# Kernel optimization log

Hardware: AMD Instinct MI355X
Metric: run time of the kernel (lower is better)

Reference implementation:

```python
import jax, jax.numpy as jnp
import numpy as np

RES = 512
N_LAYERS = 3
BATCH = 128
NUM_CLASSES = 10
LAMBDA = 5.32e-07
K = 2.0 * np.pi / LAMBDA  # module-level constant k in the original code
Z = 0.035                 # propagation distance d
DX = 1e-06                # pixel pitch


def _transfer_function(res):
    # Angular-spectrum Fresnel transfer function H(fx, fy), static numpy precompute.
    fx = np.fft.fftfreq(res, DX)
    FX, FY = np.meshgrid(fx, fx)
    H = np.exp(1j * K * Z) * np.exp(-1j * np.pi * LAMBDA * Z * (FX ** 2 + FY ** 2))
    return jnp.asarray(H.astype(np.complex64))


def setup_inputs() -> dict:
    key = jax.random.key(0)
    k1, k2, k3, k4 = jax.random.split(key, 4)
    x = jax.random.normal(k1, (BATCH, 1, RES, RES), dtype=jnp.float32)
    phases = jax.random.normal(k2, (N_LAYERS, RES, RES), dtype=jnp.float32) * 0.1
    fc_w = jax.random.normal(k3, (NUM_CLASSES, RES * RES), dtype=jnp.float32) * 0.01
    fc_b = jax.random.normal(k4, (NUM_CLASSES,), dtype=jnp.float32) * 0.01
    return {"x": x, "phases": phases, "fc_w": fc_w, "fc_b": fc_b}


def reference(x, phases, fc_w, fc_b):
    res = x.shape[-1]
    H = _transfer_function(res)  # (res, res) complex64
    field = x[:, 0].astype(jnp.complex64)  # (B, res, res)
    for i in range(phases.shape[0]):
        # phase-mask multiply, then Fresnel propagation: ifft2(fft2(field) * H)
        field = field * jnp.exp(1j * phases[i])
        field = jnp.fft.ifft2(jnp.fft.fft2(field, axes=(-2, -1)) * H, axes=(-2, -1))
    intensity = field.real ** 2 + field.imag ** 2  # |field|^2
    feat = intensity.reshape(x.shape[0], -1)
    return feat @ fc_w.T + fc_b
```

## Files before the change

### kernel.cpp

```cpp
#include <hip/hip_runtime.h>
#include <math.h>


#define PAD(i) ((i) + ((i) >> 4))
#define LSTR 545
#define PSTR 545

typedef __attribute__((ext_vector_type(2))) _Float16 half2v;
typedef __attribute__((ext_vector_type(8))) _Float16 half8;

__device__ __forceinline__ void wave_lds_order() {
  asm volatile("" ::: "memory");
}

__device__ __forceinline__ float2 cadd(float2 a, float2 b){ return make_float2(a.x+b.x, a.y+b.y); }
__device__ __forceinline__ float2 csub(float2 a, float2 b){ return make_float2(a.x-b.x, a.y-b.y); }
__device__ __forceinline__ float2 cmul(float2 a, float2 b){ return make_float2(a.x*b.x - a.y*b.y, a.x*b.y + a.y*b.x); }

template<int S>
__device__ __forceinline__ float2 cmul_s(float2 a, float2 b) {
  return (S < 0) ? make_float2(a.x*b.x - a.y*b.y, a.x*b.y + a.y*b.x)
                 : make_float2(a.x*b.x + a.y*b.y, a.y*b.x - a.x*b.y);
}

template<int S>
__device__ __forceinline__ float2 crot(float2 z){
  return (S > 0) ? make_float2(-z.y, z.x) : make_float2(z.y, -z.x);
}

template<int S>
__device__ __forceinline__ void fft8(float2 v[8]) {
  const float sq = 0.70710678118654752440f;
  float2 t0 = cadd(v[0], v[4]), t1 = csub(v[0], v[4]);
  float2 t2 = cadd(v[2], v[6]), t3 = csub(v[2], v[6]);
  float2 E0 = cadd(t0, t2), E2 = csub(t0, t2);
  float2 rt3 = crot<S>(t3);
  float2 E1 = cadd(t1, rt3), E3 = csub(t1, rt3);
  float2 u0 = cadd(v[1], v[5]), u1 = csub(v[1], v[5]);
  float2 u2 = cadd(v[3], v[7]), u3 = csub(v[3], v[7]);
  float2 O0 = cadd(u0, u2), O2 = csub(u0, u2);
  float2 ru3 = crot<S>(u3);
  float2 O1 = cadd(u1, ru3), O3 = csub(u1, ru3);
  float2 O1w = make_float2(sq*(O1.x - (float)S*O1.y), sq*((float)S*O1.x + O1.y));
  float2 O2w = crot<S>(O2);
  float2 O3w = make_float2(-sq*(O3.x + (float)S*O3.y), sq*((float)S*O3.x - O3.y));
  v[0] = cadd(E0, O0);  v[4] = csub(E0, O0);
  v[1] = cadd(E1, O1w); v[5] = csub(E1, O1w);
  v[2] = cadd(E2, O2w); v[6] = csub(E2, O2w);
  v[3] = cadd(E3, O3w); v[7] = csub(E3, O3w);
}

__device__ __forceinline__ void mktw(float2 tw2[7], float2 tw3[7], int t) {
  float a2 = -6.28318530717958647692f * (float)(t & 7) / 64.0f;
  float a3 = -6.28318530717958647692f * (float)(t & 63) / 512.0f;
  float s2, c2; __sincosf(a2, &s2, &c2);
  float s3, c3; __sincosf(a3, &s3, &c3);
  float2 w2 = make_float2(c2, s2), w3 = make_float2(c3, s3);
  tw2[0] = w2; tw3[0] = w3;
  #pragma unroll
  for (int r = 1; r < 7; ++r) { tw2[r] = cmul(tw2[r-1], w2); tw3[r] = cmul(tw3[r-1], w3); }
}

template<int S>
__device__ __forceinline__ void fft512_w(float2 v[8], float2* __restrict__ B, int t,
                                         const float2 tw2[7], const float2 tw3[7]) {
  fft8<S>(v);
  #pragma unroll
  for (int r = 0; r < 8; ++r) B[PAD(8*t + r)] = v[r];
  wave_lds_order();
  #pragma unroll
  for (int r = 0; r < 8; ++r) v[r] = B[PAD(t + 64*r)];
  #pragma unroll
  for (int r = 1; r < 8; ++r) v[r] = cmul_s<S>(v[r], tw2[r-1]);
  fft8<S>(v);
  int d = ((t >> 3) << 6) | (t & 7);
  #pragma unroll
  for (int r = 0; r < 8; ++r) B[PAD(d + 8*r)] = v[r];
  wave_lds_order();
  #pragma unroll
  for (int r = 0; r < 8; ++r) v[r] = B[PAD(t + 64*r)];
  #pragma unroll
  for (int r = 1; r < 8; ++r) v[r] = cmul_s<S>(v[r], tw3[r-1]);
  fft8<S>(v);
}

template<int S>
__device__ __forceinline__ void fft512_pair(float2 vA[8], float2 vB[8],
                                            float4* __restrict__ B, int t,
                                            const float2 tw2[7], const float2 tw3[7]) {
  fft8<S>(vA); fft8<S>(vB);
  #pragma unroll
  for (int r = 0; r < 8; ++r)
    B[PAD(8*t + r)] = make_float4(vA[r].x, vA[r].y, vB[r].x, vB[r].y);
  wave_lds_order();
  #pragma unroll
  for (int r = 0; r < 8; ++r) {
    float4 w = B[PAD(t + 64*r)];
    vA[r] = make_float2(w.x, w.y); vB[r] = make_float2(w.z, w.w);
  }
  #pragma unroll
  for (int r = 1; r < 8; ++r) {
    vA[r] = cmul_s<S>(vA[r], tw2[r-1]); vB[r] = cmul_s<S>(vB[r], tw2[r-1]);
  }
  fft8<S>(vA); fft8<S>(vB);
  int d = ((t >> 3) << 6) | (t & 7);
  #pragma unroll
  for (int r = 0; r < 8; ++r)
    B[PAD(d + 8*r)] = make_float4(vA[r].x, vA[r].y, vB[r].x, vB[r].y);
  wave_lds_order();
  #pragma unroll
  for (int r = 0; r < 8; ++r) {
    float4 w = B[PAD(t + 64*r)];
    vA[r] = make_float2(w.x, w.y); vB[r] = make_float2(w.z, w.w);
  }
  #pragma unroll
  for (int r = 1; r < 8; ++r) {
    vA[r] = cmul_s<S>(vA[r], tw3[r-1]); vB[r] = cmul_s<S>(vB[r], tw3[r-1]);
  }
  fft8<S>(vA); fft8<S>(vB);
}

__device__ __forceinline__ float2 h2f(half2v h) { return make_float2((float)h[0], (float)h[1]); }
__device__ __forceinline__ half2v f2h(float2 v) { half2v h; h[0] = (_Float16)v.x; h[1] = (_Float16)v.y; return h; }


__global__ __launch_bounds__(256) void k_hinit(float2* __restrict__ hx,
                                               float2* __restrict__ hy) {
  int idx = blockIdx.x * 256 + threadIdx.x;
  int u = idx & 511;
  double f = (double)(u < 256 ? u : u - 512) * 1953.125;
  const double LAM = 5.32e-7, ZD = 0.035;
  const double PI = 3.14159265358979323846;
  double s, c;
  if (idx < 512) {
    double ang = -PI * LAM * ZD * f * f;
    sincos(ang, &s, &c);
    hx[u] = make_float2((float)c, (float)s);
  } else {
    double ang = (2.0 * PI / LAM) * ZD - PI * LAM * ZD * f * f;
    sincos(ang, &s, &c);
    const double sc = 1.0 / 262144.0;
    hy[u] = make_float2((float)(c * sc), (float)(s * sc));
  }
}

__global__ __launch_bounds__(256) void k_r1(const float* __restrict__ x,
                                            const float* __restrict__ ph,
                                            half2v* __restrict__ F) {
  __shared__ float2 lds[4 * LSTR];
  int tid = threadIdx.x;
  int t = tid & 63, rl = tid >> 6;
  size_t row = (size_t)blockIdx.x * 4 + rl;
  int y = (int)(row & 511);
  const float* xr = x + row * 512;
  const float* pr = ph + (size_t)y * 512;
  float2 tw2[7], tw3[7];
  mktw(tw2, tw3, t);
  float2 v[8];
  #pragma unroll
  for (int r = 0; r < 8; ++r) {
    int e = t + 64*r;
    float a = xr[e];
    float p = pr[e];
    float sn, cs; __sincosf(p, &sn, &cs);
    v[r] = make_float2(a * cs, a * sn);
  }
  fft512_w<-1>(v, lds + rl * LSTR, t, tw2, tw3);
  half2v* Fr = F + row * 512;
  #pragma unroll
  for (int r = 0; r < 8; ++r) Fr[t + 64*r] = f2h(v[r]);
}

__global__ __launch_bounds__(256) void k_rmid(half2v* __restrict__ F,
                                              const float* __restrict__ ph) {
  __shared__ float2 lds[4 * LSTR];
  int tid = threadIdx.x;
  int t = tid & 63, rl = tid >> 6;
  size_t row = (size_t)blockIdx.x * 4 + rl;
  int y = (int)(row & 511);
  half2v* Fr = F + row * 512;
  const float* pr = ph + (size_t)y * 512;
  float pv[8];
  #pragma unroll
  for (int r = 0; r < 8; ++r) pv[r] = pr[t + 64*r];
  float2 tw2[7], tw3[7];
  mktw(tw2, tw3, t);
  float2 v[8];
  #pragma unroll
  for (int r = 0; r < 8; ++r) v[r] = h2f(Fr[t + 64*r]);
  fft512_w<1>(v, lds + rl * LSTR, t, tw2, tw3);
  #pragma unroll
  for (int r = 0; r < 8; ++r) {
    float sn, cs; __sincosf(pv[r], &sn, &cs);
    v[r] = cmul(v[r], make_float2(cs, sn));
  }
  fft512_w<-1>(v, lds + rl * LSTR, t, tw2, tw3);
  #pragma unroll
  for (int r = 0; r < 8; ++r) Fr[t + 64*r] = f2h(v[r]);
}

__global__ __launch_bounds__(512) void k_col(half2v* __restrict__ F,
                                             const float2* __restrict__ hx,
                                             const float2* __restrict__ hy) {
  __shared__ float4 lds[8 * PSTR];
  int b = blockIdx.x >> 5;
  int x0 = (blockIdx.x & 31) << 4;
  half2v* Fb = F + (size_t)b * 262144;
  half8* Fb8 = (half8*)Fb;
  int tid = threadIdx.x;
  int t = tid & 63, cl = tid >> 6;
  float2 hyv[8];
  #pragma unroll
  for (int r = 0; r < 8; ++r) hyv[r] = hy[t + 64*r];
  float2 hxA = hx[x0 + 2*cl], hxB = hx[x0 + 2*cl + 1];
  float2 tw2[7], tw3[7];
  mktw(tw2, tw3, t);
  #pragma unroll
  for (int i = 0; i < 4; ++i) {
    int f = tid + 512 * i;
    int yy = f >> 2, c4 = f & 3;
    half8 d = Fb8[(size_t)yy * 128 + (x0 >> 2) + c4];
    int pb = PAD(yy);
    lds[(2*c4)     * PSTR + pb] = make_float4((float)d[0], (float)d[1],
                                              (float)d[2], (float)d[3]);
    lds[(2*c4 + 1) * PSTR + pb] = make_float4((float)d[4], (float)d[5],
                                              (float)d[6], (float)d[7]);
  }
  __syncthreads();
  float4* B = lds + cl * PSTR;
  float2 vA[8], vB[8];
  #pragma unroll
  for (int r = 0; r < 8; ++r) {
    float4 w = B[PAD(t + 64*r)];
    vA[r] = make_float2(w.x, w.y); vB[r] = make_float2(w.z, w.w);
  }
  fft512_pair<-1>(vA, vB, B, t, tw2, tw3);
  #pragma unroll
  for (int r = 0; r < 8; ++r) {
    vA[r] = cmul(cmul(vA[r], hyv[r]), hxA);
    vB[r] = cmul(cmul(vB[r], hyv[r]), hxB);
  }
  fft512_pair<1>(vA, vB, B, t, tw2, tw3);
  #pragma unroll
  for (int r = 0; r < 8; ++r)
    B[PAD(t + 64*r)] = make_float4(vA[r].x, vA[r].y, vB[r].x, vB[r].y);
  __syncthreads();
  #pragma unroll
  for (int i = 0; i < 4; ++i) {
    int f = tid + 512 * i;
    int yy = f >> 2, c4 = f & 3;
    int pb = PAD(yy);
    float4 a  = lds[(2*c4)     * PSTR + pb];
    float4 bb = lds[(2*c4 + 1) * PSTR + pb];
    half8 o;
    o[0] = (_Float16)a.x;  o[1] = (_Float16)a.y;
    o[2] = (_Float16)a.z;  o[3] = (_Float16)a.w;
    o[4] = (_Float16)bb.x; o[5] = (_Float16)bb.y;
    o[6] = (_Float16)bb.z; o[7] = (_Float16)bb.w;
    Fb8[(size_t)yy * 128 + (x0 >> 2) + c4] = o;
  }
}

__global__ __launch_bounds__(256) void k_rlast(const half2v* __restrict__ F,
                                               const float* __restrict__ W,
                                               float* __restrict__ partial, int m) {
  __shared__ float2 lds[4 * LSTR];
  int tid = threadIdx.x;
  int t = tid & 63, rl = tid >> 6;
  int nq = (m + 3) >> 2;
  int y = blockIdx.x / nq;
  int q = blockIdx.x - y * nq;
  int g = q * 4 + rl;
  bool act = (g < m);
  const half2v* Fr = F + ((size_t)g * 262144 + (size_t)y * 512);
  float2 tw2[7], tw3[7];
  mktw(tw2, tw3, t);
  float2 v[8];
  #pragma unroll
  for (int r = 0; r < 8; ++r) {
    half2v h = act ? Fr[t + 64*r] : (half2v)(_Float16)0.0f;
    v[r] = h2f(h);
  }
  fft512_w<1>(v, lds + rl * LSTR, t, tw2, tw3);
  float acc[10];
  #pragma unroll
  for (int c = 0; c < 10; ++c) acc[c] = 0.0f;
  const float* Wy = W + (size_t)y * 512;
  #pragma unroll
  for (int r = 0; r < 8; ++r) {
    int e = t + 64*r;
    float I = v[r].x * v[r].x + v[r].y * v[r].y;
    #pragma unroll
    for (int c = 0; c < 10; ++c) acc[c] += I * Wy[(size_t)c * 262144 + e];
  }
  float mine = 0.0f;
  #pragma unroll
  for (int c = 0; c < 10; ++c) {
    float s = acc[c];
    #pragma unroll
    for (int off = 32; off > 0; off >>= 1) s += __shfl_xor(s, off, 64);
    if (t == c) mine = s;
  }
  if (act && t < 10)
    partial[((size_t)g * 10 + t) * 512 + y] = mine;
}

__global__ __launch_bounds__(64) void k_fc(const float* __restrict__ partial,
                                           const float* __restrict__ fc_b,
                                           float* __restrict__ out, int b0, int m) {
  int bid = blockIdx.x;
  int g = bid / 10, c = bid - g * 10;
  int t = threadIdx.x;
  const float* p = partial + ((size_t)g * 10 + c) * 512;
  float s = 0.0f;
  #pragma unroll
  for (int r = 0; r < 8; ++r) s += p[t + 64*r];
  #pragma unroll
  for (int off = 32; off > 0; off >>= 1) s += __shfl_xor(s, off, 64);
  if (t == 0) out[(size_t)(b0 + g) * 10 + c] = s + fc_b[c];
}


extern "C" void kernel_launch(void* const* d_in, const int* in_sizes, int n_in,
                              void* d_out, int out_size, void* d_ws, size_t ws_size,
                              hipStream_t stream) {
  const float* x    = (const float*)d_in[0];
  const float* ph   = (const float*)d_in[1];
  const float* fc_w = (const float*)d_in[2];
  const float* fc_b = (const float*)d_in[3];
  float* out = (float*)d_out;

  const size_t IMG = 262144;
  const size_t PER_IMG = IMG * sizeof(half2v) + 512 * 10 * sizeof(float);
  float2* hx = (float2*)d_ws;
  float2* hy = hx + 512;
  size_t avail = (ws_size > IMG * sizeof(float2)) ? ws_size - IMG * sizeof(float2) : 0;
  int M = (int)(avail / PER_IMG);
  if (M < 1) M = 1;
  if (M > 128) M = 128;
  half2v* F  = (half2v*)((char*)d_ws + IMG * sizeof(float2));
  float* part = (float*)((char*)F + (size_t)M * IMG * sizeof(half2v));

  hipLaunchKernelGGL(k_hinit, dim3(4), dim3(256), 0, stream, hx, hy);

  for (int b0 = 0; b0 < 128; b0 += M) {
    int m = (128 - b0 < M) ? (128 - b0) : M;
    int rblocks = m * 128;
    int cblocks = m * 32;
    int nq = (m + 3) >> 2;
    hipLaunchKernelGGL(k_r1,    dim3(rblocks), dim3(256), 0, stream, x + (size_t)b0 * IMG, ph, F);
    hipLaunchKernelGGL(k_col,   dim3(cblocks), dim3(512), 0, stream, F, (const float2*)hx, (const float2*)hy);
    hipLaunchKernelGGL(k_rmid,  dim3(rblocks), dim3(256), 0, stream, F, ph + IMG);
    hipLaunchKernelGGL(k_col,   dim3(cblocks), dim3(512), 0, stream, F, (const float2*)hx, (const float2*)hy);
    hipLaunchKernelGGL(k_rmid,  dim3(rblocks), dim3(256), 0, stream, F, ph + 2 * IMG);
    hipLaunchKernelGGL(k_col,   dim3(cblocks), dim3(512), 0, stream, F, (const float2*)hx, (const float2*)hy);
    hipLaunchKernelGGL(k_rlast, dim3(512 * nq), dim3(256), 0, stream, F, fc_w, part, m);
    hipLaunchKernelGGL(k_fc,    dim3(m * 10), dim3(64), 0, stream, part, fc_b, out, b0, m);
  }
}
```

Baseline: 784.1 us.

## Make column FFT kernel persistent with register prefetch of next tile

The column-pass kernel now launches a capped grid of at most 512 blocks that loop over tiles in grid-stride order. Each block loads the next tile's half8 data into registers while it transforms the current tile, overlapping global loads with the FFT work, and twiddles and hy are set up once per block. In exchange it holds more registers for the prefetch buffer, adds an extra barrier per tile, and runs fewer blocks at once, which may lower the occupancy available to hide latency.

New measurement: 695.5 us. 1.13x faster.

```diff
diff --git a/kernel.cpp b/kernel.cpp
--- a/kernel.cpp
+++ b/kernel.cpp
@@ -201,63 +201,90 @@
 
 __global__ __launch_bounds__(512) void k_col(half2v* __restrict__ F,
                                              const float2* __restrict__ hx,
-                                             const float2* __restrict__ hy) {
+                                             const float2* __restrict__ hy,
+                                             int ntiles) {
   __shared__ float4 lds[8 * PSTR];
-  int b = blockIdx.x >> 5;
-  int x0 = (blockIdx.x & 31) << 4;
-  half2v* Fb = F + (size_t)b * 262144;
-  half8* Fb8 = (half8*)Fb;
   int tid = threadIdx.x;
   int t = tid & 63, cl = tid >> 6;
   float2 hyv[8];
   #pragma unroll
   for (int r = 0; r < 8; ++r) hyv[r] = hy[t + 64*r];
-  float2 hxA = hx[x0 + 2*cl], hxB = hx[x0 + 2*cl + 1];
   float2 tw2[7], tw3[7];
   mktw(tw2, tw3, t);
-  #pragma unroll
-  for (int i = 0; i < 4; ++i) {
-    int f = tid + 512 * i;
-    int yy = f >> 2, c4 = f & 3;
-    half8 d = Fb8[(size_t)yy * 128 + (x0 >> 2) + c4];
-    int pb = PAD(yy);
-    lds[(2*c4)     * PSTR + pb] = make_float4((float)d[0], (float)d[1],
-                                              (float)d[2], (float)d[3]);
-    lds[(2*c4 + 1) * PSTR + pb] = make_float4((float)d[4], (float)d[5],
-                                              (float)d[6], (float)d[7]);
-  }
-  __syncthreads();
-  float4* B = lds + cl * PSTR;
-  float2 vA[8], vB[8];
-  #pragma unroll
-  for (int r = 0; r < 8; ++r) {
-    float4 w = B[PAD(t + 64*r)];
-    vA[r] = make_float2(w.x, w.y); vB[r] = make_float2(w.z, w.w);
-  }
-  fft512_pair<-1>(vA, vB, B, t, tw2, tw3);
-  #pragma unroll
-  for (int r = 0; r < 8; ++r) {
-    vA[r] = cmul(cmul(vA[r], hyv[r]), hxA);
-    vB[r] = cmul(cmul(vB[r], hyv[r]), hxB);
-  }
-  fft512_pair<1>(vA, vB, B, t, tw2, tw3);
-  #pragma unroll
-  for (int r = 0; r < 8; ++r)
-    B[PAD(t + 64*r)] = make_float4(vA[r].x, vA[r].y, vB[r].x, vB[r].y);
-  __syncthreads();
-  #pragma unroll
-  for (int i = 0; i < 4; ++i) {
-    int f = tid + 512 * i;
-    int yy = f >> 2, c4 = f & 3;
-    int pb = PAD(yy);
-    float4 a  = lds[(2*c4)     * PSTR + pb];
-    float4 bb = lds[(2*c4 + 1) * PSTR + pb];
-    half8 o;
-    o[0] = (_Float16)a.x;  o[1] = (_Float16)a.y;
-    o[2] = (_Float16)a.z;  o[3] = (_Float16)a.w;
-    o[4] = (_Float16)bb.x; o[5] = (_Float16)bb.y;
-    o[6] = (_Float16)bb.z; o[7] = (_Float16)bb.w;
-    Fb8[(size_t)yy * 128 + (x0 >> 2) + c4] = o;
+
+  int tile = blockIdx.x;
+  half8 pf[4];
+  if (tile < ntiles) {
+    int b = tile >> 5, x0 = (tile & 31) << 4;
+    const half8* Fb8 = (const half8*)(F + (size_t)b * 262144);
+    #pragma unroll
+    for (int i = 0; i < 4; ++i) {
+      int f = tid + 512 * i;
+      int yy = f >> 2, c4 = f & 3;
+      pf[i] = Fb8[(size_t)yy * 128 + (x0 >> 2) + c4];
+    }
+  }
+  while (tile < ntiles) {
+    int b = tile >> 5, x0 = (tile & 31) << 4;
+    half8* Fb8 = (half8*)(F + (size_t)b * 262144);
+    float2 hxA = hx[x0 + 2*cl], hxB = hx[x0 + 2*cl + 1];
+    #pragma unroll
+    for (int i = 0; i < 4; ++i) {
+      int f = tid + 512 * i;
+      int yy = f >> 2, c4 = f & 3;
+      half8 d = pf[i];
+      int pb = PAD(yy);
+      lds[(2*c4)     * PSTR + pb] = make_float4((float)d[0], (float)d[1],
+                                                (float)d[2], (float)d[3]);
+      lds[(2*c4 + 1) * PSTR + pb] = make_float4((float)d[4], (float)d[5],
+                                                (float)d[6], (float)d[7]);
+    }
+    int next = tile + (int)gridDim.x;
+    if (next < ntiles) {
+      int nb = next >> 5, nx0 = (next & 31) << 4;
+      const half8* Nb8 = (const half8*)(F + (size_t)nb * 262144);
+      #pragma unroll
+      for (int i = 0; i < 4; ++i) {
+        int f = tid + 512 * i;
+        int yy = f >> 2, c4 = f & 3;
+        pf[i] = Nb8[(size_t)yy * 128 + (nx0 >> 2) + c4];
+      }
+    }
+    __syncthreads();
+    float4* B = lds + cl * PSTR;
+    float2 vA[8], vB[8];
+    #pragma unroll
+    for (int r = 0; r < 8; ++r) {
+      float4 w = B[PAD(t + 64*r)];
+      vA[r] = make_float2(w.x, w.y); vB[r] = make_float2(w.z, w.w);
+    }
+    fft512_pair<-1>(vA, vB, B, t, tw2, tw3);
+    #pragma unroll
+    for (int r = 0; r < 8; ++r) {
+      vA[r] = cmul(cmul(vA[r], hyv[r]), hxA);
+      vB[r] = cmul(cmul(vB[r], hyv[r]), hxB);
+    }
+    fft512_pair<1>(vA, vB, B, t, tw2, tw3);
+    #pragma unroll
+    for (int r = 0; r < 8; ++r)
+      B[PAD(t + 64*r)] = make_float4(vA[r].x, vA[r].y, vB[r].x, vB[r].y);
+    __syncthreads();
+    #pragma unroll
+    for (int i = 0; i < 4; ++i) {
+      int f = tid + 512 * i;
+      int yy = f >> 2, c4 = f & 3;
+      int pb = PAD(yy);
+      float4 a  = lds[(2*c4)     * PSTR + pb];
+      float4 bb = lds[(2*c4 + 1) * PSTR + pb];
+      half8 o;
+      o[0] = (_Float16)a.x;  o[1] = (_Float16)a.y;
+      o[2] = (_Float16)a.z;  o[3] = (_Float16)a.w;
+      o[4] = (_Float16)bb.x; o[5] = (_Float16)bb.y;
+      o[6] = (_Float16)bb.z; o[7] = (_Float16)bb.w;
+      Fb8[(size_t)yy * 128 + (x0 >> 2) + c4] = o;
+    }
+    __syncthreads();
+    tile = next;
   }
 }
 
@@ -346,14 +373,15 @@
   for (int b0 = 0; b0 < 128; b0 += M) {
     int m = (128 - b0 < M) ? (128 - b0) : M;
     int rblocks = m * 128;
-    int cblocks = m * 32;
+    int ntiles = m * 32;
+    int cgrid = ntiles < 512 ? ntiles : 512;
     int nq = (m + 3) >> 2;
     hipLaunchKernelGGL(k_r1,    dim3(rblocks), dim3(256), 0, stream, x + (size_t)b0 * IMG, ph, F);
-    hipLaunchKernelGGL(k_col,   dim3(cblocks), dim3(512), 0, stream, F, (const float2*)hx, (const float2*)hy);
+    hipLaunchKernelGGL(k_col,   dim3(cgrid), dim3(512), 0, stream, F, (const float2*)hx, (const float2*)hy, ntiles);
     hipLaunchKernelGGL(k_rmid,  dim3(rblocks), dim3(256), 0, stream, F, ph + IMG);
-    hipLaunchKernelGGL(k_col,   dim3(cblocks), dim3(512), 0, stream, F, (const float2*)hx, (const float2*)hy);
+    hipLaunchKernelGGL(k_col,   dim3(cgrid), dim3(512), 0, stream, F, (const float2*)hx, (const float2*)hy, ntiles);
     hipLaunchKernelGGL(k_rmid,  dim3(rblocks), dim3(256), 0, stream, F, ph + 2 * IMG);
-    hipLaunchKernelGGL(k_col,   dim3(cblocks), dim3(512), 0, stream, F, (const float2*)hx, (const float2*)hy);
+    hipLaunchKernelGGL(k_col,   dim3(cgrid), dim3(512), 0, stream, F, (const float2*)hx, (const float2*)hy, ntiles);
     hipLaunchKernelGGL(k_rlast, dim3(512 * nq), dim3(256), 0, stream, F, fc_w, part, m);
     hipLaunchKernelGGL(k_fc,    dim3(m * 10), dim3(64), 0, stream, part, fc_b, out, b0, m);
   }
```

## Replace column FFT kernel with transposed ping-pong buffers and persistent prefetching kernels

Applied to the files above, without the earlier changes.

Each row kernel now writes its result transposed via an LDS tile into a second buffer, so the column pass becomes a contiguous row-style FFT (k_cmid) instead of a strided gather of 16-column tiles. Kernels become persistent grid-stride loops over groups of 8 rows, with register prefetch of the next group's inputs to overlap loads with FFT compute. The 1/N normalization is split between hy and an explicit 1/512 scale to keep fp16 intermediates in range. This costs double workspace (A/B buffers), which lowers the batch chunk size M, and adds three block-wide syncs per group for the transpose.

Measured after the change: 796.8 us. No clear change (+1.6%).

```diff
diff --git a/kernel.cpp b/kernel.cpp
--- a/kernel.cpp
+++ b/kernel.cpp
@@ -4,7 +4,6 @@
 
 #define PAD(i) ((i) + ((i) >> 4))
 #define LSTR 545
-#define PSTR 545
 
 typedef __attribute__((ext_vector_type(2))) _Float16 half2v;
 typedef __attribute__((ext_vector_type(8))) _Float16 half8;
@@ -84,44 +83,26 @@
   fft8<S>(v);
 }
 
-template<int S>
-__device__ __forceinline__ void fft512_pair(float2 vA[8], float2 vB[8],
-                                            float4* __restrict__ B, int t,
-                                            const float2 tw2[7], const float2 tw3[7]) {
-  fft8<S>(vA); fft8<S>(vB);
-  #pragma unroll
-  for (int r = 0; r < 8; ++r)
-    B[PAD(8*t + r)] = make_float4(vA[r].x, vA[r].y, vB[r].x, vB[r].y);
-  wave_lds_order();
-  #pragma unroll
-  for (int r = 0; r < 8; ++r) {
-    float4 w = B[PAD(t + 64*r)];
-    vA[r] = make_float2(w.x, w.y); vB[r] = make_float2(w.z, w.w);
-  }
-  #pragma unroll
-  for (int r = 1; r < 8; ++r) {
-    vA[r] = cmul_s<S>(vA[r], tw2[r-1]); vB[r] = cmul_s<S>(vB[r], tw2[r-1]);
-  }
-  fft8<S>(vA); fft8<S>(vB);
-  int d = ((t >> 3) << 6) | (t & 7);
-  #pragma unroll
-  for (int r = 0; r < 8; ++r)
-    B[PAD(d + 8*r)] = make_float4(vA[r].x, vA[r].y, vB[r].x, vB[r].y);
-  wave_lds_order();
-  #pragma unroll
-  for (int r = 0; r < 8; ++r) {
-    float4 w = B[PAD(t + 64*r)];
-    vA[r] = make_float2(w.x, w.y); vB[r] = make_float2(w.z, w.w);
-  }
-  #pragma unroll
-  for (int r = 1; r < 8; ++r) {
-    vA[r] = cmul_s<S>(vA[r], tw3[r-1]); vB[r] = cmul_s<S>(vB[r], tw3[r-1]);
-  }
-  fft8<S>(vA); fft8<S>(vB);
-}
-
 __device__ __forceinline__ float2 h2f(half2v h) { return make_float2((float)h[0], (float)h[1]); }
 __device__ __forceinline__ half2v f2h(float2 v) { half2v h; h[0] = (_Float16)v.x; h[1] = (_Float16)v.y; return h; }
+
+__device__ __forceinline__ void store_T(float2* lds, const float2 v[8],
+                                        int t, int w, int tid,
+                                        half2v* __restrict__ dst, int rowbase) {
+  __syncthreads();
+  half2v* tile = (half2v*)lds;
+  #pragma unroll
+  for (int r = 0; r < 8; ++r) tile[w * 512 + t + 64*r] = f2h(v[r]);
+  __syncthreads();
+  int j = tid;
+  half2v seg[8];
+  #pragma unroll
+  for (int w2 = 0; w2 < 8; ++w2) seg[w2] = tile[w2 * 512 + j];
+  float4* d4 = (float4*)(dst + (size_t)j * 512 + rowbase);
+  d4[0] = *(float4*)&seg[0];
+  d4[1] = *(float4*)&seg[4];
+  __syncthreads();
+}
 
 
 __global__ __launch_bounds__(256) void k_hinit(float2* __restrict__ hx,
@@ -139,125 +120,137 @@
   } else {
     double ang = (2.0 * PI / LAM) * ZD - PI * LAM * ZD * f * f;
     sincos(ang, &s, &c);
-    const double sc = 1.0 / 262144.0;
+    const double sc = 1.0 / 512.0;
     hy[u] = make_float2((float)(c * sc), (float)(s * sc));
   }
 }
 
-__global__ __launch_bounds__(256) void k_r1(const float* __restrict__ x,
+__global__ __launch_bounds__(512) void k_r1(const float* __restrict__ x,
                                             const float* __restrict__ ph,
-                                            half2v* __restrict__ F) {
-  __shared__ float2 lds[4 * LSTR];
+                                            half2v* __restrict__ Bout, int ng) {
+  __shared__ float2 lds[8 * LSTR];
   int tid = threadIdx.x;
-  int t = tid & 63, rl = tid >> 6;
-  size_t row = (size_t)blockIdx.x * 4 + rl;
-  int y = (int)(row & 511);
-  const float* xr = x + row * 512;
-  const float* pr = ph + (size_t)y * 512;
+  int t = tid & 63, w = tid >> 6;
   float2 tw2[7], tw3[7];
   mktw(tw2, tw3, t);
-  float2 v[8];
-  #pragma unroll
-  for (int r = 0; r < 8; ++r) {
-    int e = t + 64*r;
-    float a = xr[e];
-    float p = pr[e];
-    float sn, cs; __sincosf(p, &sn, &cs);
-    v[r] = make_float2(a * cs, a * sn);
-  }
-  fft512_w<-1>(v, lds + rl * LSTR, t, tw2, tw3);
-  half2v* Fr = F + row * 512;
-  #pragma unroll
-  for (int r = 0; r < 8; ++r) Fr[t + 64*r] = f2h(v[r]);
-}
-
-__global__ __launch_bounds__(256) void k_rmid(half2v* __restrict__ F,
-                                              const float* __restrict__ ph) {
-  __shared__ float2 lds[4 * LSTR];
+  int grp = blockIdx.x;
+  float pfx[8], pfp[8];
+  if (grp < ng) {
+    size_t row = (size_t)grp * 8 + w;
+    const float* xr = x + row * 512;
+    const float* pr = ph + (size_t)(row & 511) * 512;
+    #pragma unroll
+    for (int r = 0; r < 8; ++r) { pfx[r] = xr[t + 64*r]; pfp[r] = pr[t + 64*r]; }
+  }
+  while (grp < ng) {
+    float2 v[8];
+    #pragma unroll
+    for (int r = 0; r < 8; ++r) {
+      float sn, cs; __sincosf(pfp[r], &sn, &cs);
+      v[r] = make_float2(pfx[r] * cs, pfx[r] * sn);
+    }
+    int next = grp + (int)gridDim.x;
+    if (next < ng) {
+      size_t nrow = (size_t)next * 8 + w;
+      const float* xr = x + nrow * 512;
+      const float* pr = ph + (size_t)(nrow & 511) * 512;
+      #pragma unroll
+      for (int r = 0; r < 8; ++r) { pfx[r] = xr[t + 64*r]; pfp[r] = pr[t + 64*r]; }
+    }
+    fft512_w<-1>(v, lds + w * LSTR, t, tw2, tw3);
+    int bimg = (grp * 8) >> 9, rowbase = (grp * 8) & 511;
+    store_T(lds, v, t, w, tid, Bout + (size_t)bimg * 262144, rowbase);
+    grp = next;
+  }
+}
+
+__global__ __launch_bounds__(512) void k_cmid(const half2v* __restrict__ Bin,
+                                              half2v* __restrict__ Aout,
+                                              const float2* __restrict__ hx,
+                                              const float2* __restrict__ hy,
+                                              int ng) {
+  __shared__ float2 lds[8 * LSTR];
   int tid = threadIdx.x;
-  int t = tid & 63, rl = tid >> 6;
-  size_t row = (size_t)blockIdx.x * 4 + rl;
-  int y = (int)(row & 511);
-  half2v* Fr = F + row * 512;
-  const float* pr = ph + (size_t)y * 512;
-  float pv[8];
-  #pragma unroll
-  for (int r = 0; r < 8; ++r) pv[r] = pr[t + 64*r];
+  int t = tid & 63, w = tid >> 6;
+  float2 hyv[8];
+  #pragma unroll
+  for (int r = 0; r < 8; ++r) hyv[r] = hy[t + 64*r];
   float2 tw2[7], tw3[7];
   mktw(tw2, tw3, t);
-  float2 v[8];
-  #pragma unroll
-  for (int r = 0; r < 8; ++r) v[r] = h2f(Fr[t + 64*r]);
-  fft512_w<1>(v, lds + rl * LSTR, t, tw2, tw3);
-  #pragma unroll
-  for (int r = 0; r < 8; ++r) {
-    float sn, cs; __sincosf(pv[r], &sn, &cs);
-    v[r] = cmul(v[r], make_float2(cs, sn));
-  }
-  fft512_w<-1>(v, lds + rl * LSTR, t, tw2, tw3);
-  #pragma unroll
-  for (int r = 0; r < 8; ++r) Fr[t + 64*r] = f2h(v[r]);
-}
-
-__global__ __launch_bounds__(512) void k_col(half2v* __restrict__ F,
-                                             const float2* __restrict__ hx,
-                                             const float2* __restrict__ hy) {
-  __shared__ float4 lds[8 * PSTR];
-  int b = blockIdx.x >> 5;
-  int x0 = (blockIdx.x & 31) << 4;
-  half2v* Fb = F + (size_t)b * 262144;
-  half8* Fb8 = (half8*)Fb;
+  int grp = blockIdx.x;
+  half2v pff[8];
+  if (grp < ng) {
+    int bimg = (grp * 8) >> 9, kx = (grp * 8 + w) & 511;
+    const half2v* src = Bin + (size_t)bimg * 262144 + (size_t)kx * 512;
+    #pragma unroll
+    for (int r = 0; r < 8; ++r) pff[r] = src[t + 64*r];
+  }
+  while (grp < ng) {
+    int bimg = (grp * 8) >> 9, kx = (grp * 8 + w) & 511;
+    float2 v[8];
+    #pragma unroll
+    for (int r = 0; r < 8; ++r) v[r] = h2f(pff[r]);
+    int next = grp + (int)gridDim.x;
+    if (next < ng) {
+      int nb = (next * 8) >> 9, nkx = (next * 8 + w) & 511;
+      const half2v* src = Bin + (size_t)nb * 262144 + (size_t)nkx * 512;
+      #pragma unroll
+      for (int r = 0; r < 8; ++r) pff[r] = src[t + 64*r];
+    }
+    fft512_w<-1>(v, lds + w * LSTR, t, tw2, tw3);
+    float2 hxv = hx[kx];
+    #pragma unroll
+    for (int r = 0; r < 8; ++r) v[r] = cmul(cmul(v[r], hyv[r]), hxv);
+    fft512_w<1>(v, lds + w * LSTR, t, tw2, tw3);
+    const float s512 = 1.0f / 512.0f;
+    #pragma unroll
+    for (int r = 0; r < 8; ++r) { v[r].x *= s512; v[r].y *= s512; }
+    int rowbase = (grp * 8) & 511;
+    store_T(lds, v, t, w, tid, Aout + (size_t)bimg * 262144, rowbase);
+    grp = next;
+  }
+}
+
+__global__ __launch_bounds__(512) void k_rmid(const half2v* __restrict__ Ain,
+                                              half2v* __restrict__ Bout,
+                                              const float* __restrict__ ph, int ng) {
+  __shared__ float2 lds[8 * LSTR];
   int tid = threadIdx.x;
-  int t = tid & 63, cl = tid >> 6;
-  float2 hyv[8];
-  #pragma unroll
-  for (int r = 0; r < 8; ++r) hyv[r] = hy[t + 64*r];
-  float2 hxA = hx[x0 + 2*cl], hxB = hx[x0 + 2*cl + 1];
+  int t = tid & 63, w = tid >> 6;
   float2 tw2[7], tw3[7];
   mktw(tw2, tw3, t);
-  #pragma unroll
-  for (int i = 0; i < 4; ++i) {
-    int f = tid + 512 * i;
-    int yy = f >> 2, c4 = f & 3;
-    half8 d = Fb8[(size_t)yy * 128 + (x0 >> 2) + c4];
-    int pb = PAD(yy);
-    lds[(2*c4)     * PSTR + pb] = make_float4((float)d[0], (float)d[1],
-                                              (float)d[2], (float)d[3]);
-    lds[(2*c4 + 1) * PSTR + pb] = make_float4((float)d[4], (float)d[5],
-                                              (float)d[6], (float)d[7]);
-  }
-  __syncthreads();
-  float4* B = lds + cl * PSTR;
-  float2 vA[8], vB[8];
-  #pragma unroll
-  for (int r = 0; r < 8; ++r) {
-    float4 w = B[PAD(t + 64*r)];
-    vA[r] = make_float2(w.x, w.y); vB[r] = make_float2(w.z, w.w);
-  }
-  fft512_pair<-1>(vA, vB, B, t, tw2, tw3);
-  #pragma unroll
-  for (int r = 0; r < 8; ++r) {
-    vA[r] = cmul(cmul(vA[r], hyv[r]), hxA);
-    vB[r] = cmul(cmul(vB[r], hyv[r]), hxB);
-  }
-  fft512_pair<1>(vA, vB, B, t, tw2, tw3);
-  #pragma unroll
-  for (int r = 0; r < 8; ++r)
-    B[PAD(t + 64*r)] = make_float4(vA[r].x, vA[r].y, vB[r].x, vB[r].y);
-  __syncthreads();
-  #pragma unroll
-  for (int i = 0; i < 4; ++i) {
-    int f = tid + 512 * i;
-    int yy = f >> 2, c4 = f & 3;
-    int pb = PAD(yy);
-    float4 a  = lds[(2*c4)     * PSTR + pb];
-    float4 bb = lds[(2*c4 + 1) * PSTR + pb];
-    half8 o;
-    o[0] = (_Float16)a.x;  o[1] = (_Float16)a.y;
-    o[2] = (_Float16)a.z;  o[3] = (_Float16)a.w;
-    o[4] = (_Float16)bb.x; o[5] = (_Float16)bb.y;
-    o[6] = (_Float16)bb.z; o[7] = (_Float16)bb.w;
-    Fb8[(size_t)yy * 128 + (x0 >> 2) + c4] = o;
+  int grp = blockIdx.x;
+  half2v pff[8]; float pfp[8];
+  if (grp < ng) {
+    int bimg = (grp * 8) >> 9, y = (grp * 8 + w) & 511;
+    const half2v* src = Ain + (size_t)bimg * 262144 + (size_t)y * 512;
+    const float* pr = ph + (size_t)y * 512;
+    #pragma unroll
+    for (int r = 0; r < 8; ++r) { pff[r] = src[t + 64*r]; pfp[r] = pr[t + 64*r]; }
+  }
+  while (grp < ng) {
+    int bimg = (grp * 8) >> 9;
+    float2 v[8]; float cur_p[8];
+    #pragma unroll
+    for (int r = 0; r < 8; ++r) { v[r] = h2f(pff[r]); cur_p[r] = pfp[r]; }
+    int next = grp + (int)gridDim.x;
+    if (next < ng) {
+      int nb = (next * 8) >> 9, nyy = (next * 8 + w) & 511;
+      const half2v* src = Ain + (size_t)nb * 262144 + (size_t)nyy * 512;
+      const float* pr = ph + (size_t)nyy * 512;
+      #pragma unroll
+      for (int r = 0; r < 8; ++r) { pff[r] = src[t + 64*r]; pfp[r] = pr[t + 64*r]; }
+    }
+    fft512_w<1>(v, lds + w * LSTR, t, tw2, tw3);
+    #pragma unroll
+    for (int r = 0; r < 8; ++r) {
+      float sn, cs; __sincosf(cur_p[r], &sn, &cs);
+      v[r] = cmul(v[r], make_float2(cs, sn));
+    }
+    fft512_w<-1>(v, lds + w * LSTR, t, tw2, tw3);
+    int rowbase = (grp * 8) & 511;
+    store_T(lds, v, t, w, tid, Bout + (size_t)bimg * 262144, rowbase);
+    grp = next;
   }
 }
 
@@ -331,30 +324,39 @@
   float* out = (float*)d_out;
 
   const size_t IMG = 262144;
-  const size_t PER_IMG = IMG * sizeof(half2v) + 512 * 10 * sizeof(float);
+  const size_t PER_IMG = 2 * IMG * sizeof(half2v) + 512 * 10 * sizeof(float);
   float2* hx = (float2*)d_ws;
   float2* hy = hx + 512;
-  size_t avail = (ws_size > IMG * sizeof(float2)) ? ws_size - IMG * sizeof(float2) : 0;
+  size_t hdr = 1024 * sizeof(float2);
+  size_t avail = (ws_size > hdr) ? ws_size - hdr : 0;
   int M = (int)(avail / PER_IMG);
   if (M < 1) M = 1;
   if (M > 128) M = 128;
-  half2v* F  = (half2v*)((char*)d_ws + IMG * sizeof(float2));
-  float* part = (float*)((char*)F + (size_t)M * IMG * sizeof(half2v));
+  half2v* A = (half2v*)((char*)d_ws + hdr);
+  half2v* B = A + (size_t)M * IMG;
+  float* part = (float*)(B + (size_t)M * IMG);
 
   hipLaunchKernelGGL(k_hinit, dim3(4), dim3(256), 0, stream, hx, hy);
 
   for (int b0 = 0; b0 < 128; b0 += M) {
     int m = (128 - b0 < M) ? (128 - b0) : M;
-    int rblocks = m * 128;
-    int cblocks = m * 32;
+    int ng = m * 64;
+    int g512 = ng < 1024 ? ng : 1024;
     int nq = (m + 3) >> 2;
-    hipLaunchKernelGGL(k_r1,    dim3(rblocks), dim3(256), 0, stream, x + (size_t)b0 * IMG, ph, F);
-    hipLaunchKernelGGL(k_col,   dim3(cblocks), dim3(512), 0, stream, F, (const float2*)hx, (const float2*)hy);
-    hipLaunchKernelGGL(k_rmid,  dim3(rblocks), dim3(256), 0, stream, F, ph + IMG);
-    hipLaunchKernelGGL(k_col,   dim3(cblocks), dim3(512), 0, stream, F, (const float2*)hx, (const float2*)hy);
-    hipLaunchKernelGGL(k_rmid,  dim3(rblocks), dim3(256), 0, stream, F, ph + 2 * IMG);
-    hipLaunchKernelGGL(k_col,   dim3(cblocks), dim3(512), 0, stream, F, (const float2*)hx, (const float2*)hy);
-    hipLaunchKernelGGL(k_rlast, dim3(512 * nq), dim3(256), 0, stream, F, fc_w, part, m);
-    hipLaunchKernelGGL(k_fc,    dim3(m * 10), dim3(64), 0, stream, part, fc_b, out, b0, m);
-  }
-}
+    hipLaunchKernelGGL(k_r1,   dim3(g512), dim3(512), 0, stream,
+                       x + (size_t)b0 * IMG, ph, B, ng);
+    hipLaunchKernelGGL(k_cmid, dim3(g512), dim3(512), 0, stream,
+                       (const half2v*)B, A, (const float2*)hx, (const float2*)hy, ng);
+    hipLaunchKernelGGL(k_rmid, dim3(g512), dim3(512), 0, stream,
+                       (const half2v*)A, B, ph + IMG, ng);
+    hipLaunchKernelGGL(k_cmid, dim3(g512), dim3(512), 0, stream,
+                       (const half2v*)B, A, (const float2*)hx, (const float2*)hy, ng);
+    hipLaunchKernelGGL(k_rmid, dim3(g512), dim3(512), 0, stream,
+                       (const half2v*)A, B, ph + 2 * IMG, ng);
+    hipLaunchKernelGGL(k_cmid, dim3(g512), dim3(512), 0, stream,
+                       (const half2v*)B, A, (const float2*)hx, (const float2*)hy, ng);
+    hipLaunchKernelGGL(k_rlast, dim3(512 * nq), dim3(256), 0, stream,
+                       (const half2v*)A, fc_w, part, m);
+    hipLaunchKernelGGL(k_fc,   dim3(m * 10), dim3(64), 0, stream, part, fc_b, out, b0, m);
+  }
+}
```
